# Kernel tuning notes

Hardware: AMD Instinct MI355X
Metric: run time of the kernel (lower is better)

The kernel has to match this reference:

```python
import jax, jax.numpy as jnp
import numpy as np

B, TV, TS, D = 16, 256, 32, 512


def setup_inputs() -> dict:
    key = jax.random.key(0)
    ks = jax.random.split(key, 8)
    return {
        "video_feature": jax.random.normal(ks[0], (B, TV, D), dtype=jnp.float32),
        "video_mask": jnp.ones((B, TV), dtype=jnp.float32),
        "sentence_feature": jax.random.normal(ks[1], (B, TS, D), dtype=jnp.float32),
        "sentence_mask": jnp.ones((B, TS), dtype=jnp.float32),
        "w1": jax.random.normal(ks[2], (D, D), dtype=jnp.float32) * (1.0 / np.sqrt(D)),
        "b1": jax.random.normal(ks[3], (D,), dtype=jnp.float32) * 0.02,
        "w2": jax.random.normal(ks[4], (D, D), dtype=jnp.float32) * (1.0 / np.sqrt(D)),
        "wt": jax.random.normal(ks[5], (D,), dtype=jnp.float32) * (1.0 / np.sqrt(D)),
    }


def reference(video_feature, video_mask, sentence_feature, sentence_mask, w1, b1, w2, wt):
    # tmp1: [B, Tv, D] masked video projection (Linear with bias)
    tmp1 = (jnp.einsum("bvd,ed->bve", video_feature, w1) + b1) * video_mask[:, :, None]
    # tmp2: [B, Ts, D] masked sentence projection (Linear, no bias)
    tmp2 = jnp.einsum("bsd,ed->bse", sentence_feature, w2) * sentence_mask[:, :, None]
    # pairwise mask: [B, Tv, Ts]
    pair_mask = video_mask[:, :, None] * sentence_mask[:, None, :]
    # broadcast-add -> [B, Tv, Ts, D], mask, tanh, reduce with wt -> [B, Tv, Ts]
    tmp = (tmp1[:, :, None, :] + tmp2[:, None, :, :]) * pair_mask[..., None]
    M = jnp.einsum("bvsd,d->bvs", jnp.tanh(tmp), wt)
    return M * pair_mask
```

## Files before the change

### kernel.cpp

```cpp
#include <hip/hip_runtime.h>

#define BB 16
#define TV 256
#define TS 32
#define DD 512

typedef float    floatx4  __attribute__((ext_vector_type(4)));
typedef short    short8   __attribute__((ext_vector_type(8)));
typedef unsigned short ushort8 __attribute__((ext_vector_type(8)));

#define TANH_SCALE 2.885390082f

static __device__ __forceinline__ unsigned short f2bf(float f) {
    unsigned int u = __float_as_uint(f);
    u += 0x7FFFu + ((u >> 16) & 1u);
    return (unsigned short)(u >> 16);
}

__global__ __launch_bounds__(256) void ta_convert(
    const float* __restrict__ video, const float* __restrict__ sent,
    const float* __restrict__ w1,    const float* __restrict__ w2,
    unsigned short* __restrict__ vb, unsigned short* __restrict__ sb,
    unsigned short* __restrict__ w1b, unsigned short* __restrict__ w2b)
{
    const int NV = BB * TV * DD, NS = BB * TS * DD, NW = DD * DD;
    const int base = (blockIdx.x * 256 + threadIdx.x) * 8;
    const float* src; unsigned short* dst; int off;
    if      (base < NV)           { src = video; dst = vb;  off = base; }
    else if (base < NV + NS)      { src = sent;  dst = sb;  off = base - NV; }
    else if (base < NV + NS + NW) { src = w1;    dst = w1b; off = base - NV - NS; }
    else                          { src = w2;    dst = w2b; off = base - NV - NS - NW; }
    const float4 a = *(const float4*)(src + off);
    const float4 b = *(const float4*)(src + off + 4);
    ushort8 o;
    o[0] = f2bf(a.x); o[1] = f2bf(a.y); o[2] = f2bf(a.z); o[3] = f2bf(a.w);
    o[4] = f2bf(b.x); o[5] = f2bf(b.y); o[6] = f2bf(b.z); o[7] = f2bf(b.w);
    *(ushort8*)(dst + off) = o;
}

__global__ __launch_bounds__(256) void ta_mfma_gemm(
    const unsigned short* __restrict__ vb, const unsigned short* __restrict__ w1b,
    const float* __restrict__ b1,          const float* __restrict__ vmask,
    float* __restrict__ tmp1e,
    const unsigned short* __restrict__ sb, const unsigned short* __restrict__ w2b,
    const float* __restrict__ smask,       float* __restrict__ tmp2e,
    const float* __restrict__ wt,          float* __restrict__ wsum)
{
    const int t = threadIdx.x;

    if (blockIdx.x == 0 && t < 64) {
        float v = 0.f;
        for (int i = t; i < DD; i += 64) v += wt[i];
        for (int off = 32; off; off >>= 1) v += __shfl_down(v, off);
        if (t == 0) wsum[0] = v;
    }

    const bool g2 = (blockIdx.x >= 512);
    const int bid = g2 ? (int)blockIdx.x - 512 : (int)blockIdx.x;
    const unsigned short* __restrict__ A = g2 ? sb    : vb;
    const unsigned short* __restrict__ W = g2 ? w2b   : w1b;
    const float* __restrict__ rm         = g2 ? smask : vmask;
    const int m0 = (g2 ? (bid & 7)  : (bid & 63)) * 64;
    const int n0 = (g2 ? (bid >> 3) : (bid >> 6)) * 64;

    __shared__ unsigned short As[2][4096];
    __shared__ unsigned short Bs[2][4096];

    const int lane = t & 63;
    const int wid  = t >> 6;
    const int wm   = wid >> 1, wn = wid & 1;
    const int lr   = lane & 15, kg = lane >> 4;

    const int r0 = t >> 3,          g0c = (t & 7) ^ (r0 & 7);
    const int r1 = (t + 256) >> 3,  g1c = (t & 7) ^ (r1 & 7);
    const unsigned short* a0p = A + (size_t)(m0 + r0) * DD + g0c * 8;
    const unsigned short* a1p = A + (size_t)(m0 + r1) * DD + g1c * 8;
    const unsigned short* w0p = W + (size_t)(n0 + r0) * DD + g0c * 8;
    const unsigned short* w1p = W + (size_t)(n0 + r1) * DD + g1c * 8;
    const int l0 = t * 8;
    const int l1 = (t + 256) * 8;

#define TA_STAGE(buf, koff) do {                                               \
    __builtin_amdgcn_global_load_lds(                                          \
        (const __attribute__((address_space(1))) void*)(a0p + (koff)),         \
        (__attribute__((address_space(3))) void*)&As[buf][l0], 16, 0, 0);      \
    __builtin_amdgcn_global_load_lds(                                          \
        (const __attribute__((address_space(1))) void*)(a1p + (koff)),         \
        (__attribute__((address_space(3))) void*)&As[buf][l1], 16, 0, 0);      \
    __builtin_amdgcn_global_load_lds(                                          \
        (const __attribute__((address_space(1))) void*)(w0p + (koff)),         \
        (__attribute__((address_space(3))) void*)&Bs[buf][l0], 16, 0, 0);      \
    __builtin_amdgcn_global_load_lds(                                          \
        (const __attribute__((address_space(1))) void*)(w1p + (koff)),         \
        (__attribute__((address_space(3))) void*)&Bs[buf][l1], 16, 0, 0);      \
  } while (0)

    floatx4 acc[2][2] = {};

    const int ml0 = wm * 32 + lr, ml1 = ml0 + 16;
    const int nl0 = wn * 32 + lr, nl1 = nl0 + 16;
    const int sa0 = ml0 * 64, sa1 = ml1 * 64;
    const int sb0 = nl0 * 64, sb1 = nl1 * 64;
    const int xa = ml0 & 7, xb = nl0 & 7;

    TA_STAGE(0, 0);
    __syncthreads();

    int cur = 0;
    for (int step = 0; step < 8; ++step) {
        if (step < 7) TA_STAGE(cur ^ 1, (step + 1) * 64);
#pragma unroll
        for (int kk = 0; kk < 2; ++kk) {
            const int kc = kk * 4 + kg;
            short8 a0 = *(const short8*)&As[cur][sa0 + ((kc ^ xa) << 3)];
            short8 a1 = *(const short8*)&As[cur][sa1 + ((kc ^ xa) << 3)];
            short8 b0 = *(const short8*)&Bs[cur][sb0 + ((kc ^ xb) << 3)];
            short8 b1 = *(const short8*)&Bs[cur][sb1 + ((kc ^ xb) << 3)];
            acc[0][0] = __builtin_amdgcn_mfma_f32_16x16x32_bf16(a0, b0, acc[0][0], 0, 0, 0);
            acc[0][1] = __builtin_amdgcn_mfma_f32_16x16x32_bf16(a0, b1, acc[0][1], 0, 0, 0);
            acc[1][0] = __builtin_amdgcn_mfma_f32_16x16x32_bf16(a1, b0, acc[1][0], 0, 0, 0);
            acc[1][1] = __builtin_amdgcn_mfma_f32_16x16x32_bf16(a1, b1, acc[1][1], 0, 0, 0);
        }
        __syncthreads();
        cur ^= 1;
    }
#undef TA_STAGE

#pragma unroll
    for (int fm = 0; fm < 2; ++fm)
#pragma unroll
        for (int fn = 0; fn < 2; ++fn)
#pragma unroll
            for (int r = 0; r < 4; ++r) {
                const int m = m0 + wm * 32 + fm * 16 + kg * 4 + r;
                const int n = n0 + wn * 32 + fn * 16 + lr;
                const float mk = rm[m] * TANH_SCALE;
                const float val = acc[fm][fn][r];
                if (!g2) {
                    tmp1e[(size_t)m * DD + n] =
                        __builtin_amdgcn_exp2f((val + b1[n]) * mk);
                } else {
                    tmp2e[(size_t)(m >> 5) * DD * TS + (size_t)n * TS + (m & 31)] =
                        __builtin_amdgcn_exp2f(val * mk);
                }
            }
}

__global__ __launch_bounds__(512) void ta_tanh_main(
    const float* __restrict__ tmp1e,
    const float* __restrict__ tmp2e,
    const float* __restrict__ wt,
    const float* __restrict__ wsum,
    const float* __restrict__ vmask,
    const float* __restrict__ smask,
    float* __restrict__ out)
{
    __shared__ float t2s[DD * TS];
    __shared__ float e1s[4 * DD];
    __shared__ float part[512];

    const int t  = threadIdx.x;
    const int b  = blockIdx.x >> 6;
    const int v0 = (blockIdx.x & 63) << 2;

    {
        const float4* src = (const float4*)(tmp2e + (size_t)b * DD * TS);
        float4* dst = (float4*)t2s;
#pragma unroll
        for (int i = 0; i < 8; ++i) dst[t + 512 * i] = src[t + 512 * i];
        const int c = t * 4, row = c >> 9, col = c & 511;
        *(float4*)&e1s[c] =
            *(const float4*)&tmp1e[(size_t)(b * TV + v0 + row) * DD + col];
    }
    __syncthreads();

    const int s  = t & 31;
    const int vi = (t >> 5) & 3;
    const int q  = __builtin_amdgcn_readfirstlane(t >> 7);

    const float* __restrict__ e1p = e1s + vi * DD + q * 128;
    const float* __restrict__ wtp = wt + q * 128;
    const int tbase = q * 4096 + s;

    floatx4 acc4a = {0.f, 0.f, 0.f, 0.f};
    floatx4 acc4b = {0.f, 0.f, 0.f, 0.f};
#pragma unroll 2
    for (int i = 0; i < 16; ++i) {
        floatx4 e1a = *(const floatx4*)(e1p + i * 8);
        floatx4 e1b = *(const floatx4*)(e1p + i * 8 + 4);
        floatx4 wa  = *(const floatx4*)(wtp + i * 8);
        floatx4 wb  = *(const floatx4*)(wtp + i * 8 + 4);
        const int dof = tbase + i * 256;
        float e20 = t2s[dof];        float e21 = t2s[dof + 32];
        float e22 = t2s[dof + 64];   float e23 = t2s[dof + 96];
        float e24 = t2s[dof + 128];  float e25 = t2s[dof + 160];
        float e26 = t2s[dof + 192];  float e27 = t2s[dof + 224];
        floatx4 da = { e1a[0] * e20 + 1.f, e1a[1] * e21 + 1.f,
                       e1a[2] * e22 + 1.f, e1a[3] * e23 + 1.f };
        floatx4 db = { e1b[0] * e24 + 1.f, e1b[1] * e25 + 1.f,
                       e1b[2] * e26 + 1.f, e1b[3] * e27 + 1.f };
        floatx4 ra = { __builtin_amdgcn_rcpf(da[0]), __builtin_amdgcn_rcpf(da[1]),
                       __builtin_amdgcn_rcpf(da[2]), __builtin_amdgcn_rcpf(da[3]) };
        floatx4 rb = { __builtin_amdgcn_rcpf(db[0]), __builtin_amdgcn_rcpf(db[1]),
                       __builtin_amdgcn_rcpf(db[2]), __builtin_amdgcn_rcpf(db[3]) };
        acc4a = acc4a + wa * ra;
        acc4b = acc4b + wb * rb;
    }

    part[t] = (acc4a[0] + acc4a[1]) + (acc4a[2] + acc4a[3])
            + (acc4b[0] + acc4b[1]) + (acc4b[2] + acc4b[3]);
    __syncthreads();

    if (t < 128) {
        const float sum = part[t] + part[t + 128] + part[t + 256] + part[t + 384];
        const int s2 = t & 31, vi2 = t >> 5;
        const int v2 = v0 + vi2;
        const float pm2 = vmask[b * TV + v2] * smask[b * TS + s2];
        out[((size_t)b * TV + v2) * TS + s2] = pm2 * (wsum[0] - 2.f * sum);
    }
}

extern "C" void kernel_launch(void* const* d_in, const int* in_sizes, int n_in,
                              void* d_out, int out_size, void* d_ws, size_t ws_size,
                              hipStream_t stream)
{
    const float* video = (const float*)d_in[0];
    const float* vmask = (const float*)d_in[1];
    const float* sent  = (const float*)d_in[2];
    const float* smask = (const float*)d_in[3];
    const float* w1    = (const float*)d_in[4];
    const float* b1    = (const float*)d_in[5];
    const float* w2    = (const float*)d_in[6];
    const float* wt    = (const float*)d_in[7];
    float* out = (float*)d_out;

    const size_t NV = (size_t)BB * TV * DD, NS = (size_t)BB * TS * DD, NW = (size_t)DD * DD;

    float* tmp1e         = (float*)d_ws;
    float* tmp2e         = tmp1e + NV;
    unsigned short* vb   = (unsigned short*)(tmp2e + NS);
    unsigned short* sb   = vb + NV;
    unsigned short* w1b  = sb + NS;
    unsigned short* w2b  = w1b + NW;
    float* wsum          = (float*)(w2b + NW);

    const int total8 = (int)((NV + NS + 2 * NW) / 8);
    ta_convert<<<dim3(total8 / 256), dim3(256), 0, stream>>>(
        video, sent, w1, w2, vb, sb, w1b, w2b);
    ta_mfma_gemm<<<dim3(512 + 64), dim3(256), 0, stream>>>(
        vb, w1b, b1, vmask, tmp1e, sb, w2b, smask, tmp2e, wt, wsum);
    ta_tanh_main<<<dim3(BB * (TV / 4)), dim3(512), 0, stream>>>(
        tmp1e, tmp2e, wt, wsum, vmask, smask, out);
}
```

Baseline: 37.05 us.

## Store tmp2 exp in bf16 pairs and share one reciprocal across two video rows

The sentence-side exponentials are now stored as bf16, packed in pairs along D, which halves the shared-memory footprint and the global traffic for the tanh stage. Each thread now handles two video rows (8 per block instead of 4) and computes both reciprocals from a single rcp of the product of the two denominators. This trades two rcp instructions for one rcp plus a few multiplies, and halves the block count. Exponent inputs are clamped to avoid overflow in the product. The cost is reduced precision in the tmp2 factor and possible overflow or precision loss when multiplying the two denominators.

```diff
diff --git a/kernel.cpp b/kernel.cpp
--- a/kernel.cpp
+++ b/kernel.cpp
@@ -43,7 +43,7 @@
     const float* __restrict__ b1,          const float* __restrict__ vmask,
     float* __restrict__ tmp1e,
     const unsigned short* __restrict__ sb, const unsigned short* __restrict__ w2b,
-    const float* __restrict__ smask,       float* __restrict__ tmp2e,
+    const float* __restrict__ smask,       unsigned short* __restrict__ tmp2h,
     const float* __restrict__ wt,          float* __restrict__ wsum)
 {
     const int t = threadIdx.x;
@@ -135,88 +135,110 @@
                 const int m = m0 + wm * 32 + fm * 16 + kg * 4 + r;
                 const int n = n0 + wn * 32 + fn * 16 + lr;
                 const float mk = rm[m] * TANH_SCALE;
-                const float val = acc[fm][fn][r];
+                float z = g2 ? (acc[fm][fn][r] * mk)
+                             : (acc[fm][fn][r] + b1[n]) * mk;
+                z = fminf(fmaxf(z, -30.f), 30.f);
+                const float e = __builtin_amdgcn_exp2f(z);
                 if (!g2) {
-                    tmp1e[(size_t)m * DD + n] =
-                        __builtin_amdgcn_exp2f((val + b1[n]) * mk);
+                    tmp1e[(size_t)m * DD + n] = e;
                 } else {
-                    tmp2e[(size_t)(m >> 5) * DD * TS + (size_t)n * TS + (m & 31)] =
-                        __builtin_amdgcn_exp2f(val * mk);
+                    tmp2h[(size_t)(m >> 5) * 16384 + (size_t)(n >> 1) * 64
+                          + (m & 31) * 2 + (n & 1)] = f2bf(e);
                 }
             }
 }
 
-__global__ __launch_bounds__(512) void ta_tanh_main(
+__global__ __launch_bounds__(512, 4) void ta_tanh_main(
     const float* __restrict__ tmp1e,
-    const float* __restrict__ tmp2e,
+    const unsigned short* __restrict__ tmp2h,
     const float* __restrict__ wt,
     const float* __restrict__ wsum,
     const float* __restrict__ vmask,
     const float* __restrict__ smask,
     float* __restrict__ out)
 {
-    __shared__ float t2s[DD * TS];
-    __shared__ float e1s[4 * DD];
-    __shared__ float part[512];
+    __shared__ unsigned int t2u[8192];
+    __shared__ float e1s[8 * DD];
+    __shared__ float part[1024];
 
     const int t  = threadIdx.x;
-    const int b  = blockIdx.x >> 6;
-    const int v0 = (blockIdx.x & 63) << 2;
+    const int b  = blockIdx.x >> 5;
+    const int v0 = (blockIdx.x & 31) << 3;
 
     {
-        const float4* src = (const float4*)(tmp2e + (size_t)b * DD * TS);
-        float4* dst = (float4*)t2s;
-#pragma unroll
-        for (int i = 0; i < 8; ++i) dst[t + 512 * i] = src[t + 512 * i];
-        const int c = t * 4, row = c >> 9, col = c & 511;
-        *(float4*)&e1s[c] =
-            *(const float4*)&tmp1e[(size_t)(b * TV + v0 + row) * DD + col];
+        const ushort8* src = (const ushort8*)(tmp2h + (size_t)b * 16384);
+        ushort8* dst = (ushort8*)t2u;
+#pragma unroll
+        for (int i = 0; i < 4; ++i) dst[t + 512 * i] = src[t + 512 * i];
+#pragma unroll
+        for (int i = 0; i < 2; ++i) {
+            const int c = t + 512 * i;
+            const int row = c >> 7, col = (c & 127) << 2;
+            *(float4*)&e1s[row * DD + col] =
+                *(const float4*)&tmp1e[(size_t)(b * TV + v0 + row) * DD + col];
+        }
     }
     __syncthreads();
 
     const int s  = t & 31;
     const int vi = (t >> 5) & 3;
-    const int q  = __builtin_amdgcn_readfirstlane(t >> 7);
-
-    const float* __restrict__ e1p = e1s + vi * DD + q * 128;
-    const float* __restrict__ wtp = wt + q * 128;
-    const int tbase = q * 4096 + s;
-
-    floatx4 acc4a = {0.f, 0.f, 0.f, 0.f};
-    floatx4 acc4b = {0.f, 0.f, 0.f, 0.f};
-#pragma unroll 2
+    const int q  = t >> 7;
+
+    const float* __restrict__ e1lo = e1s + vi * DD + q * 128;
+    const float* __restrict__ e1hi = e1s + (vi + 4) * DD + q * 128;
+    const float* __restrict__ wtp  = wt + q * 128;
+    const int ubase = q * 2048 + s;
+
+    floatx4 alo = {0.f, 0.f, 0.f, 0.f};
+    floatx4 ahi = {0.f, 0.f, 0.f, 0.f};
+#pragma unroll 4
     for (int i = 0; i < 16; ++i) {
-        floatx4 e1a = *(const floatx4*)(e1p + i * 8);
-        floatx4 e1b = *(const floatx4*)(e1p + i * 8 + 4);
+        const int ub = ubase + i * 128;
+        const unsigned u0 = t2u[ub];
+        const unsigned u1 = t2u[ub + 32];
+        const unsigned u2 = t2u[ub + 64];
+        const unsigned u3 = t2u[ub + 96];
+        floatx4 xl0 = *(const floatx4*)(e1lo + i * 8);
+        floatx4 xl1 = *(const floatx4*)(e1lo + i * 8 + 4);
+        floatx4 xh0 = *(const floatx4*)(e1hi + i * 8);
+        floatx4 xh1 = *(const floatx4*)(e1hi + i * 8 + 4);
         floatx4 wa  = *(const floatx4*)(wtp + i * 8);
         floatx4 wb  = *(const floatx4*)(wtp + i * 8 + 4);
-        const int dof = tbase + i * 256;
-        float e20 = t2s[dof];        float e21 = t2s[dof + 32];
-        float e22 = t2s[dof + 64];   float e23 = t2s[dof + 96];
-        float e24 = t2s[dof + 128];  float e25 = t2s[dof + 160];
-        float e26 = t2s[dof + 192];  float e27 = t2s[dof + 224];
-        floatx4 da = { e1a[0] * e20 + 1.f, e1a[1] * e21 + 1.f,
-                       e1a[2] * e22 + 1.f, e1a[3] * e23 + 1.f };
-        floatx4 db = { e1b[0] * e24 + 1.f, e1b[1] * e25 + 1.f,
-                       e1b[2] * e26 + 1.f, e1b[3] * e27 + 1.f };
-        floatx4 ra = { __builtin_amdgcn_rcpf(da[0]), __builtin_amdgcn_rcpf(da[1]),
-                       __builtin_amdgcn_rcpf(da[2]), __builtin_amdgcn_rcpf(da[3]) };
-        floatx4 rb = { __builtin_amdgcn_rcpf(db[0]), __builtin_amdgcn_rcpf(db[1]),
-                       __builtin_amdgcn_rcpf(db[2]), __builtin_amdgcn_rcpf(db[3]) };
-        acc4a = acc4a + wa * ra;
-        acc4b = acc4b + wb * rb;
-    }
-
-    part[t] = (acc4a[0] + acc4a[1]) + (acc4a[2] + acc4a[3])
-            + (acc4b[0] + acc4b[1]) + (acc4b[2] + acc4b[3]);
+        float e2[8] = {
+            __uint_as_float(u0 << 16), __uint_as_float(u0 & 0xffff0000u),
+            __uint_as_float(u1 << 16), __uint_as_float(u1 & 0xffff0000u),
+            __uint_as_float(u2 << 16), __uint_as_float(u2 & 0xffff0000u),
+            __uint_as_float(u3 << 16), __uint_as_float(u3 & 0xffff0000u)
+        };
+#pragma unroll
+        for (int j = 0; j < 4; ++j) {
+            const float dlo = fmaf(xl0[j], e2[j], 1.f);
+            const float dhi = fmaf(xh0[j], e2[j], 1.f);
+            const float inv = __builtin_amdgcn_rcpf(dlo * dhi);
+            alo[j] = fmaf(wa[j], dhi * inv, alo[j]);
+            ahi[j] = fmaf(wa[j], dlo * inv, ahi[j]);
+        }
+#pragma unroll
+        for (int j = 0; j < 4; ++j) {
+            const float dlo = fmaf(xl1[j], e2[j + 4], 1.f);
+            const float dhi = fmaf(xh1[j], e2[j + 4], 1.f);
+            const float inv = __builtin_amdgcn_rcpf(dlo * dhi);
+            alo[j] = fmaf(wb[j], dhi * inv, alo[j]);
+            ahi[j] = fmaf(wb[j], dlo * inv, ahi[j]);
+        }
+    }
+
+    part[vi * 128 + s * 4 + q]       = (alo[0] + alo[1]) + (alo[2] + alo[3]);
+    part[(vi + 4) * 128 + s * 4 + q] = (ahi[0] + ahi[1]) + (ahi[2] + ahi[3]);
     __syncthreads();
 
-    if (t < 128) {
-        const float sum = part[t] + part[t + 128] + part[t + 256] + part[t + 384];
-        const int s2 = t & 31, vi2 = t >> 5;
-        const int v2 = v0 + vi2;
-        const float pm2 = vmask[b * TV + v2] * smask[b * TS + s2];
-        out[((size_t)b * TV + v2) * TS + s2] = pm2 * (wsum[0] - 2.f * sum);
+    if (t < 256) {
+        const int sv = t >> 5, s2 = t & 31;
+        const float4 p4 = *(const float4*)&part[sv * 128 + s2 * 4];
+        const float sum = (p4.x + p4.y) + (p4.z + p4.w);
+        const int v = v0 + sv;
+        const float pm = vmask[b * TV + v] * smask[b * TS + s2];
+        out[((size_t)b * TV + v) * TS + s2] = pm * (wsum[0] - 2.f * sum);
     }
 }
 
@@ -237,8 +259,8 @@
     const size_t NV = (size_t)BB * TV * DD, NS = (size_t)BB * TS * DD, NW = (size_t)DD * DD;
 
     float* tmp1e         = (float*)d_ws;
-    float* tmp2e         = tmp1e + NV;
-    unsigned short* vb   = (unsigned short*)(tmp2e + NS);
+    unsigned short* tmp2h = (unsigned short*)(tmp1e + NV);
+    unsigned short* vb   = tmp2h + NS;
     unsigned short* sb   = vb + NV;
     unsigned short* w1b  = sb + NS;
     unsigned short* w2b  = w1b + NW;
@@ -248,7 +270,7 @@
     ta_convert<<<dim3(total8 / 256), dim3(256), 0, stream>>>(
         video, sent, w1, w2, vb, sb, w1b, w2b);
     ta_mfma_gemm<<<dim3(512 + 64), dim3(256), 0, stream>>>(
-        vb, w1b, b1, vmask, tmp1e, sb, w2b, smask, tmp2e, wt, wsum);
-    ta_tanh_main<<<dim3(BB * (TV / 4)), dim3(512), 0, stream>>>(
-        tmp1e, tmp2e, wt, wsum, vmask, smask, out);
-}
+        vb, w1b, b1, vmask, tmp1e, sb, w2b, smask, tmp2h, wt, wsum);
+    ta_tanh_main<<<dim3(BB * (TV / 8)), dim3(512), 0, stream>>>(
+        tmp1e, tmp2h, wt, wsum, vmask, smask, out);
+}
```

Measured after the change: 36.44 us. About the same (-1.6%).
